# Kernel optimization log

Hardware: AMD Instinct MI355X
Metric: run time of the kernel (lower is better)

The kernel has to match this reference:

```python
import jax, jax.numpy as jnp
import numpy as np

N_HEADS = 16


def setup_inputs() -> dict:
    # ALiBi slopes: 2^(-h * 8/n_heads) for h = 1..n_heads (deterministic buffer)
    h = jnp.arange(1, N_HEADS + 1, dtype=jnp.float32)
    slopes = jnp.power(2.0, -h * (8.0 / N_HEADS))
    return {"slopes": slopes, "seq_len": 4096}


def reference(slopes, seq_len):
    # distance[i, j] = |i - j|
    pos = jnp.arange(seq_len, dtype=jnp.float32)
    dist = jnp.abs(pos[:, None] - pos[None, :])                 # [S, S]
    # bias[h, i, j] = -slope[h] * dist[i, j]
    bias = -slopes[:, None, None] * dist[None, :, :]            # [H, S, S]
    # causal mask: zero out past/current (j <= i), keep future (j > i)
    future = pos[None, :] > pos[:, None]                        # strictly upper triangle
    return bias * future[None, :, :].astype(bias.dtype)
```

## Files before the change

kernel.cpp:

```cpp
#include <hip/hip_runtime.h>


#define ALIBI_S 4096
#define ALIBI_H 16

__global__ __launch_bounds__(256) void alibi_bias_kernel(
    const float* __restrict__ slopes,
    float4* __restrict__ out,
    unsigned int n4)
{
    const unsigned int stride = gridDim.x * blockDim.x;
    for (unsigned int t = blockIdx.x * blockDim.x + threadIdx.x; t < n4; t += stride) {
        const unsigned int e = t << 2;
        const int h = (int)(e >> 24);
        const int i = (int)((e >> 12) & 4095);
        const int j = (int)(e & 4095);
        const float ns = -slopes[h];

        float4 v;
        v.x = (j + 0 > i) ? ns * (float)(j + 0 - i) : 0.0f;
        v.y = (j + 1 > i) ? ns * (float)(j + 1 - i) : 0.0f;
        v.z = (j + 2 > i) ? ns * (float)(j + 2 - i) : 0.0f;
        v.w = (j + 3 > i) ? ns * (float)(j + 3 - i) : 0.0f;
        out[t] = v;
    }
}

extern "C" void kernel_launch(void* const* d_in, const int* in_sizes, int n_in,
                              void* d_out, int out_size, void* d_ws, size_t ws_size,
                              hipStream_t stream) {
    const float* slopes = (const float*)d_in[0];
    float4* out = (float4*)d_out;

    const unsigned int n4 = (unsigned int)((unsigned long long)ALIBI_H * ALIBI_S * ALIBI_S / 4);
    const int block = 256;
    const int grid = 2048;

    alibi_bias_kernel<<<grid, block, 0, stream>>>(slopes, out, n4);
}
```

Baseline: 202.1 us.

## Use 2D grid per head with unrolled nontemporal vector stores

Replaces the grid-stride loop with a 2D grid in which blockIdx.y selects the head, so each block loads one slope and writes 16 unrolled float4 stores. Stores use __builtin_nontemporal_store to stream the 1 GiB output past the caches. This removes the per-element head index decode and the repeated slope load, and launches many more blocks (1024 x 16) for a purely write-bandwidth-bound kernel. The cost is that occupancy and tail behaviour now depend on the fixed launch shape instead of a persistent grid.

```diff
diff --git a/kernel.cpp b/kernel.cpp
--- a/kernel.cpp
+++ b/kernel.cpp
@@ -3,26 +3,35 @@
 
 #define ALIBI_S 4096
 #define ALIBI_H 16
+#define UNROLL  16
+#define BLOCK   256
 
-__global__ __launch_bounds__(256) void alibi_bias_kernel(
+typedef float f32x4 __attribute__((ext_vector_type(4)));
+
+__global__ __launch_bounds__(BLOCK) void alibi_bias_kernel(
     const float* __restrict__ slopes,
-    float4* __restrict__ out,
-    unsigned int n4)
+    f32x4* __restrict__ out)
 {
-    const unsigned int stride = gridDim.x * blockDim.x;
-    for (unsigned int t = blockIdx.x * blockDim.x + threadIdx.x; t < n4; t += stride) {
-        const unsigned int e = t << 2;
-        const int h = (int)(e >> 24);
-        const int i = (int)((e >> 12) & 4095);
-        const int j = (int)(e & 4095);
-        const float ns = -slopes[h];
+    const int h = blockIdx.y;
+    const float ns = -slopes[h];
 
-        float4 v;
+    const unsigned int base_f4 = blockIdx.x * (BLOCK * UNROLL) + threadIdx.x;
+    f32x4* plane = out + ((size_t)h << 22);
+
+#pragma unroll
+    for (int k = 0; k < UNROLL; ++k) {
+        const unsigned int f = base_f4 + (unsigned int)k * BLOCK;
+        const unsigned int e = f << 2;
+        const int i = (int)(e >> 12);
+        const int j = (int)(e & 4095u);
+
+        f32x4 v;
         v.x = (j + 0 > i) ? ns * (float)(j + 0 - i) : 0.0f;
         v.y = (j + 1 > i) ? ns * (float)(j + 1 - i) : 0.0f;
         v.z = (j + 2 > i) ? ns * (float)(j + 2 - i) : 0.0f;
         v.w = (j + 3 > i) ? ns * (float)(j + 3 - i) : 0.0f;
-        out[t] = v;
+
+        __builtin_nontemporal_store(v, plane + f);
     }
 }
 
@@ -30,11 +39,8 @@
                               void* d_out, int out_size, void* d_ws, size_t ws_size,
                               hipStream_t stream) {
     const float* slopes = (const float*)d_in[0];
-    float4* out = (float4*)d_out;
+    f32x4* out = (f32x4*)d_out;
 
-    const unsigned int n4 = (unsigned int)((unsigned long long)ALIBI_H * ALIBI_S * ALIBI_S / 4);
-    const int block = 256;
-    const int grid = 2048;
-
-    alibi_bias_kernel<<<grid, block, 0, stream>>>(slopes, out, n4);
+    dim3 grid(ALIBI_S * ALIBI_S / 4 / (BLOCK * UNROLL), ALIBI_H);
+    alibi_bias_kernel<<<grid, BLOCK, 0, stream>>>(slopes, out);
 }
```

Result: slower. 218.4 us (+8.1%).
